# Performance work log

Measured on AMD Instinct MI355X. Metric: run time of the kernel, lower is better.

## Reference

```python
import jax, jax.numpy as jnp
import numpy as np

INPUT_DIMS = 512
OUTPUT_DIMS = 512
GRID_SIZE = 8


def setup_inputs() -> dict:
    key = jax.random.key(0)
    k_x, k_w = jax.random.split(key)
    x = jax.random.normal(k_x, (4, 2048, INPUT_DIMS), dtype=jnp.float32)
    scale = 1.0 / (np.sqrt(INPUT_DIMS) * np.sqrt(GRID_SIZE))
    fouriercoeffs = jax.random.normal(
        k_w, (2, OUTPUT_DIMS, INPUT_DIMS, GRID_SIZE), dtype=jnp.float32) * scale
    bias = jnp.zeros((1, OUTPUT_DIMS), dtype=jnp.float32)
    return {"x": x, "fouriercoeffs": fouriercoeffs, "bias": bias}


def reference(x, fouriercoeffs, bias):
    out_shape = x.shape[:-1] + (OUTPUT_DIMS,)
    xf = x.reshape(-1, INPUT_DIMS)  # [N, I]
    k = jnp.arange(1, GRID_SIZE + 1, dtype=x.dtype)  # [G]
    arg = xf[:, :, None] * k  # [N, I, G]
    # contract cos/sin features against coeffs: two batched GEMMs
    y = jnp.einsum('nig,oig->no', jnp.cos(arg), fouriercoeffs[0])
    y = y + jnp.einsum('nig,oig->no', jnp.sin(arg), fouriercoeffs[1])
    y = y + bias
    return y.reshape(out_shape)
```

## Files before the change

### kernel.cpp

```cpp
#include <hip/hip_runtime.h>
#include <hip/hip_bf16.h>


typedef __attribute__((ext_vector_type(8)))  short s16x8;
typedef __attribute__((ext_vector_type(4)))  int   i32x4;
typedef __attribute__((ext_vector_type(4)))  float f32x4;
typedef __attribute__((ext_vector_type(16))) float f32x16;

#define NROWS 8192
#define IDIM  512
#define ODIM  512
#define KDIM  8192

static __device__ __forceinline__ short f2bf(float f) {
    union { float f; unsigned u; } v; v.f = f;
    unsigned r = v.u + 0x7fffu + ((v.u >> 16) & 1u);
    return (short)(r >> 16);
}

static __device__ __forceinline__ float bf2f(short h) {
    union { unsigned u; float f; } v;
    v.u = ((unsigned)(unsigned short)h) << 16;
    return v.f;
}

static __device__ __forceinline__ int pkbf(float c, float s) {
    union { __hip_bfloat162 h; int i; } u;
    u.h = __float22bfloat162_rn(make_float2(c, s));
    return u.i;
}

__global__ __launch_bounds__(256) void fkan_prep(const float* __restrict__ cf,
                                                 short* __restrict__ Wb) {
    const int o = blockIdx.x;
    const int tid = threadIdx.x;
#pragma unroll
    for (int rep = 0; rep < 2; ++rep) {
        const int i = tid + rep * 256;
        const float* c0 = cf + (o * 512 + i) * 8;
        const float* c1 = cf + ((512 + o) * 512 + i) * 8;
        float4 a0 = *(const float4*)c0;
        float4 a1 = *(const float4*)(c0 + 4);
        float4 b0 = *(const float4*)c1;
        float4 b1 = *(const float4*)(c1 + 4);
        s16x8 lo, hi;
        lo[0] = f2bf(a0.x); lo[1] = f2bf(b0.x);
        lo[2] = f2bf(a0.y); lo[3] = f2bf(b0.y);
        lo[4] = f2bf(a0.z); lo[5] = f2bf(b0.z);
        lo[6] = f2bf(a0.w); lo[7] = f2bf(b0.w);
        hi[0] = f2bf(a1.x); hi[1] = f2bf(b1.x);
        hi[2] = f2bf(a1.y); hi[3] = f2bf(b1.y);
        hi[4] = f2bf(a1.z); hi[5] = f2bf(b1.z);
        hi[6] = f2bf(a1.w); hi[7] = f2bf(b1.w);
        *(s16x8*)(Wb + o * KDIM + i * 16)     = lo;
        *(s16x8*)(Wb + o * KDIM + i * 16 + 8) = hi;
    }
}

__global__ __launch_bounds__(256, 2) void fkan_gemm10(const float* __restrict__ x,
                                                      const short* __restrict__ Wb,
                                                      short* __restrict__ P) {
    __shared__ short As[2][64 * 64];
    __shared__ short Bs[2][128 * 64];

    const int bid = blockIdx.x;
    const int xcd = bid & 7;
    const int bn = xcd & 1, kc = xcd >> 1;
    const int bm = bid >> 3;
    const int n0 = bm * 128, o0 = bn * 256, i0 = kc * 128;
    const int kbase = i0 * 16;
    const int NKT = 64;

    const int tid = threadIdx.x;
    const int wid = tid >> 6, lane = tid & 63;
    const int l32 = lane & 31, hi32 = lane >> 5;
    const int wr = wid >> 1, wc = wid & 1;

    f32x16 acc[2][4];
#pragma unroll
    for (int a = 0; a < 2; ++a)
#pragma unroll
        for (int b = 0; b < 4; ++b)
#pragma unroll
            for (int e = 0; e < 16; ++e) acc[a][b][e] = 0.f;

    const int nl = tid >> 1, isel = tid & 1;
    const float* xrow = x + (n0 + nl) * 512 + i0 + isel;

    auto stage = [&](int t, int nb, float xx) {
#pragma unroll
        for (int w = 0; w < 4; ++w) {
            const int ch = w * 256 + tid;
            const int l = ch >> 3, sl = ch & 7;
            const int cb = sl ^ (l & 7);
            const int r = 2 * l + (cb >> 2);
            const short* src = Wb + (size_t)(o0 + r) * KDIM + kbase + t * 32 + (cb & 3) * 8;
            short* ldst = &Bs[nb][w * 2048 + wid * 512];
            __builtin_amdgcn_global_load_lds(
                (const __attribute__((address_space(1))) void*)src,
                (__attribute__((address_space(3))) void*)ldst, 16, 0, 0);
        }
        float s1, c1;
        __sincosf(xx, &s1, &c1);
        float c = c1, s = s1;
        i32x4 lo, hi;
#pragma unroll
        for (int g = 0; g < 8; ++g) {
            const int p = pkbf(c, s);
            if (g < 4) lo[g] = p; else hi[g - 4] = p;
            const float t1 = s * s1, t2 = c * s1;
            const float cn = __builtin_fmaf(c, c1, -t1);
            s = __builtin_fmaf(s, c1, t2);
            c = cn;
        }
        short* Ab = As[nb];
        const int lA = nl >> 1;
        const int cb0 = (nl & 1) * 4 + isel * 2;
        *(i32x4*)&Ab[lA * 64 + ((cb0 ^ (lA & 7))) * 8]       = lo;
        *(i32x4*)&Ab[lA * 64 + (((cb0 + 1) ^ (lA & 7))) * 8] = hi;
    };

    float xv = xrow[0];
    stage(0, 0, xv);
    xv = xrow[2];
    __syncthreads();

    for (int kt = 0; kt < NKT; ++kt) {
        const int cur = kt & 1;

        s16x8 af[2][2], bfr[4][2];
#pragma unroll
        for (int mt = 0; mt < 2; ++mt)
#pragma unroll
            for (int ks = 0; ks < 2; ++ks) {
                const int row = wr * 64 + mt * 32 + l32;
                const int cch = ks * 2 + hi32;
                const int l = row >> 1;
                const int slot = (((row & 1) * 4 + cch) ^ (l & 7));
                af[mt][ks] = *(const s16x8*)&As[cur][l * 64 + slot * 8];
            }
#pragma unroll
        for (int nt = 0; nt < 4; ++nt)
#pragma unroll
            for (int ks = 0; ks < 2; ++ks) {
                const int row = wc * 128 + nt * 32 + l32;
                const int cch = ks * 2 + hi32;
                const int l = row >> 1;
                const int slot = (((row & 1) * 4 + cch) ^ (l & 7));
                bfr[nt][ks] = *(const s16x8*)&Bs[cur][l * 64 + slot * 8];
            }

        if (kt + 1 < NKT) {
            stage(kt + 1, cur ^ 1, xv);
            if (kt + 2 < NKT) xv = xrow[(kt + 2) * 2];
        }

#pragma unroll
        for (int ks = 0; ks < 2; ++ks)
#pragma unroll
            for (int mt = 0; mt < 2; ++mt)
#pragma unroll
                for (int nt = 0; nt < 4; ++nt)
                    acc[mt][nt] = __builtin_amdgcn_mfma_f32_32x32x16_bf16(
                        af[mt][ks], bfr[nt][ks], acc[mt][nt], 0, 0, 0);

        __syncthreads();
    }

    unsigned short* dst = (unsigned short*)P + (size_t)kc * (NROWS * ODIM);
#pragma unroll
    for (int mt = 0; mt < 2; ++mt)
#pragma unroll
        for (int nt = 0; nt < 4; ++nt) {
            const f32x16 v = acc[mt][nt];
            const int oc = o0 + wc * 128 + nt * 32 + l32;
            const int rb = n0 + wr * 64 + mt * 32 + 4 * hi32;
#pragma unroll
            for (int reg = 0; reg < 16; ++reg) {
                const int row = rb + (reg & 3) + 8 * (reg >> 2);
                dst[(size_t)row * 512 + oc] = (unsigned short)f2bf(v[reg]);
            }
        }
}

__global__ __launch_bounds__(256) void fkan_combine4(const short* __restrict__ P,
                                                     const float* __restrict__ bias,
                                                     float* __restrict__ out) {
    const int total = NROWS * ODIM;
    const int stride = gridDim.x * 256 * 8;
    for (int e = (blockIdx.x * 256 + threadIdx.x) * 8; e < total; e += stride) {
        s16x8 a = *(const s16x8*)(P + e);
        s16x8 b = *(const s16x8*)(P + total + e);
        s16x8 c = *(const s16x8*)(P + 2 * total + e);
        s16x8 d = *(const s16x8*)(P + 3 * total + e);
        const int col = e & 511;
        float4 c0 = *(const float4*)(bias + col);
        float4 c1 = *(const float4*)(bias + col + 4);
        float4 r0, r1;
        r0.x = (bf2f(a[0]) + bf2f(b[0])) + (bf2f(c[0]) + bf2f(d[0])) + c0.x;
        r0.y = (bf2f(a[1]) + bf2f(b[1])) + (bf2f(c[1]) + bf2f(d[1])) + c0.y;
        r0.z = (bf2f(a[2]) + bf2f(b[2])) + (bf2f(c[2]) + bf2f(d[2])) + c0.z;
        r0.w = (bf2f(a[3]) + bf2f(b[3])) + (bf2f(c[3]) + bf2f(d[3])) + c0.w;
        r1.x = (bf2f(a[4]) + bf2f(b[4])) + (bf2f(c[4]) + bf2f(d[4])) + c1.x;
        r1.y = (bf2f(a[5]) + bf2f(b[5])) + (bf2f(c[5]) + bf2f(d[5])) + c1.y;
        r1.z = (bf2f(a[6]) + bf2f(b[6])) + (bf2f(c[6]) + bf2f(d[6])) + c1.z;
        r1.w = (bf2f(a[7]) + bf2f(b[7])) + (bf2f(c[7]) + bf2f(d[7])) + c1.w;
        *(float4*)(out + e)     = r0;
        *(float4*)(out + e + 4) = r1;
    }
}

__global__ __launch_bounds__(256, 2) void fkan_gemm_fb(const float* __restrict__ x,
                                                       const short* __restrict__ Wb,
                                                       const float* __restrict__ bias,
                                                       float* __restrict__ outp) {
    __shared__ short As[2][128 * 64];
    __shared__ short Bs[2][128 * 64];
    const int bid = blockIdx.x;
    const int xcd = bid & 7, idx = bid >> 3;
    const int bn = xcd & 3, bm = idx + (xcd >> 2) * 32;
    const int n0 = bm * 128, o0 = bn * 128;
    const int tid = threadIdx.x;
    const int wid = tid >> 6, lane = tid & 63;
    const int lrow = lane & 15, lk = lane >> 4;
    const int wr = wid >> 1, wc = wid & 1;
    f32x4 acc[4][4];
#pragma unroll
    for (int a = 0; a < 4; ++a)
#pragma unroll
        for (int b = 0; b < 4; ++b) { f32x4 z = {0,0,0,0}; acc[a][b] = z; }
    const int nl = tid >> 1, isel = tid & 1;
    const float* xrow = x + (n0 + nl) * 512 + isel * 2;
    auto stage = [&](int t, int nb, float2 xvv) {
#pragma unroll
        for (int w = 0; w < 4; ++w) {
            const int chunk = w * 256 + tid;
            const int r = chunk >> 3, pc = chunk & 7;
            const int lc = pc ^ (r & 7);
            const short* src = Wb + (o0 + r) * KDIM + t * 64 + lc * 8;
            short* ldst = &Bs[nb][w * 2048 + wid * 512];
            __builtin_amdgcn_global_load_lds(
                (const __attribute__((address_space(1))) void*)src,
                (__attribute__((address_space(3))) void*)ldst, 16, 0, 0);
        }
#pragma unroll
        for (int ii = 0; ii < 2; ++ii) {
            const float xx = ii ? xvv.y : xvv.x;
            float s1, c1; __sincosf(xx, &s1, &c1);
            float c = c1, s = s1;
            i32x4 lo, hi;
#pragma unroll
            for (int g = 0; g < 8; ++g) {
                const int p = pkbf(c, s);
                if (g < 4) lo[g] = p; else hi[g - 4] = p;
                const float t1 = s * s1, t2 = c * s1;
                const float cn = __builtin_fmaf(c, c1, -t1);
                s = __builtin_fmaf(s, c1, t2); c = cn;
            }
            const int cb0 = (isel * 2 + ii) * 2;
            *(i32x4*)&As[nb][nl * 64 + ((cb0 ^ (nl & 7))) * 8]       = lo;
            *(i32x4*)&As[nb][nl * 64 + (((cb0 + 1) ^ (nl & 7))) * 8] = hi;
        }
    };
    float2 xv = *(const float2*)xrow;
    stage(0, 0, xv);
    xv = *(const float2*)(xrow + 4);
    __syncthreads();
    for (int kt = 0; kt < 128; ++kt) {
        const int cur = kt & 1;
        s16x8 af[2][4], bfr[2][4];
#pragma unroll
        for (int ksub = 0; ksub < 2; ++ksub) {
#pragma unroll
            for (int mf = 0; mf < 4; ++mf) {
                const int row = wr * 64 + mf * 16 + lrow;
                af[ksub][mf] = *(const s16x8*)&As[cur][row * 64 + ((ksub * 4 + lk) ^ (row & 7)) * 8];
            }
#pragma unroll
            for (int nf = 0; nf < 4; ++nf) {
                const int row = wc * 64 + nf * 16 + lrow;
                bfr[ksub][nf] = *(const s16x8*)&Bs[cur][row * 64 + ((ksub * 4 + lk) ^ (row & 7)) * 8];
            }
        }
        if (kt + 1 < 128) {
            stage(kt + 1, cur ^ 1, xv);
            if (kt + 2 < 128) xv = *(const float2*)(xrow + (kt + 2) * 4);
        }
#pragma unroll
        for (int ksub = 0; ksub < 2; ++ksub)
#pragma unroll
            for (int mf = 0; mf < 4; ++mf)
#pragma unroll
                for (int nf = 0; nf < 4; ++nf)
                    acc[mf][nf] = __builtin_amdgcn_mfma_f32_16x16x32_bf16(
                        af[ksub][mf], bfr[ksub][nf], acc[mf][nf], 0, 0, 0);
        __syncthreads();
    }
#pragma unroll
    for (int nf = 0; nf < 4; ++nf) {
        const int oc = o0 + wc * 64 + nf * 16 + lrow;
        const float bv = bias[oc];
#pragma unroll
        for (int mf = 0; mf < 4; ++mf) {
            const f32x4 v = acc[mf][nf];
            const int rbase = n0 + wr * 64 + mf * 16 + lk * 4;
#pragma unroll
            for (int j = 0; j < 4; ++j)
                outp[(size_t)(rbase + j) * 512 + oc] = v[j] + bv;
        }
    }
}

extern "C" void kernel_launch(void* const* d_in, const int* in_sizes, int n_in,
                              void* d_out, int out_size, void* d_ws, size_t ws_size,
                              hipStream_t stream) {
    const float* x    = (const float*)d_in[0];
    const float* cf   = (const float*)d_in[1];
    const float* bias = (const float*)d_in[2];
    float* out = (float*)d_out;

    const size_t partial_bytes = (size_t)4 * NROWS * ODIM * 2;
    const size_t wb_bytes = (size_t)ODIM * KDIM * 2;

    if (ws_size >= partial_bytes + wb_bytes) {
        short* P  = (short*)d_ws;
        short* Wb = (short*)((char*)d_ws + partial_bytes);
        fkan_prep<<<512, 256, 0, stream>>>(cf, Wb);
        fkan_gemm10<<<512, 256, 0, stream>>>(x, Wb, P);
        fkan_combine4<<<2048, 256, 0, stream>>>(P, bias, out);
    } else {
        short* Wb = (short*)d_ws;
        fkan_prep<<<512, 256, 0, stream>>>(cf, Wb);
        fkan_gemm_fb<<<256, 256, 0, stream>>>(x, Wb, bias, out);
    }
}
```

Baseline: 96.32 us.

## Build A-operand Fourier fragments in registers via permlane swap, drop A LDS tile

Instead of computing cos/sin features cooperatively and staging them through shared memory, each lane now computes the A-operand MFMA fragments for its own rows directly in registers. It uses v_permlane32_swap to rearrange the packed bf16 values into the fragment layout. This removes the A tile from LDS along with its writes and reads. The cost is that the sincos and recurrence work is duplicated, since the two wave columns covering the same rows each redo it, and the per-iteration x loads are now strided scalar loads.

```diff
diff --git a/kernel.cpp b/kernel.cpp
--- a/kernel.cpp
+++ b/kernel.cpp
@@ -57,10 +57,9 @@
     }
 }
 
-__global__ __launch_bounds__(256, 2) void fkan_gemm10(const float* __restrict__ x,
+__global__ __launch_bounds__(256, 2) void fkan_gemm11(const float* __restrict__ x,
                                                       const short* __restrict__ Wb,
                                                       short* __restrict__ P) {
-    __shared__ short As[2][64 * 64];
     __shared__ short Bs[2][128 * 64];
 
     const int bid = blockIdx.x;
@@ -84,10 +83,9 @@
 #pragma unroll
             for (int e = 0; e < 16; ++e) acc[a][b][e] = 0.f;
 
-    const int nl = tid >> 1, isel = tid & 1;
-    const float* xrow = x + (n0 + nl) * 512 + i0 + isel;
-
-    auto stage = [&](int t, int nb, float xx) {
+    const float* xlane = x + (size_t)(n0 + wr * 64 + l32) * 512 + i0 + hi32;
+
+    auto stageB = [&](int t, int nb) {
 #pragma unroll
         for (int w = 0; w < 4; ++w) {
             const int ch = w * 256 + tid;
@@ -100,59 +98,61 @@
                 (const __attribute__((address_space(1))) void*)src,
                 (__attribute__((address_space(3))) void*)ldst, 16, 0, 0);
         }
+    };
+
+    auto buildA = [&](float xx, s16x8& f0, s16x8& f1) {
         float s1, c1;
         __sincosf(xx, &s1, &c1);
         float c = c1, s = s1;
-        i32x4 lo, hi;
+        int I[8];
 #pragma unroll
         for (int g = 0; g < 8; ++g) {
-            const int p = pkbf(c, s);
-            if (g < 4) lo[g] = p; else hi[g - 4] = p;
+            I[g] = pkbf(c, s);
             const float t1 = s * s1, t2 = c * s1;
             const float cn = __builtin_fmaf(c, c1, -t1);
             s = __builtin_fmaf(s, c1, t2);
             c = cn;
         }
-        short* Ab = As[nb];
-        const int lA = nl >> 1;
-        const int cb0 = (nl & 1) * 4 + isel * 2;
-        *(i32x4*)&Ab[lA * 64 + ((cb0 ^ (lA & 7))) * 8]       = lo;
-        *(i32x4*)&Ab[lA * 64 + (((cb0 + 1) ^ (lA & 7))) * 8] = hi;
+        i32x4 a0, a1;
+#pragma unroll
+        for (int j = 0; j < 4; ++j) {
+            int va = I[j], vb = I[j + 4];
+            asm volatile("v_permlane32_swap_b32 %0, %1" : "+v"(va), "+v"(vb));
+            a0[j] = va; a1[j] = vb;
+        }
+        f0 = *(s16x8*)&a0;
+        f1 = *(s16x8*)&a1;
     };
 
-    float xv = xrow[0];
-    stage(0, 0, xv);
-    xv = xrow[2];
+    float xv0 = xlane[0];
+    float xv1 = xlane[32 * 512];
+    stageB(0, 0);
     __syncthreads();
 
     for (int kt = 0; kt < NKT; ++kt) {
         const int cur = kt & 1;
-
-        s16x8 af[2][2], bfr[4][2];
-#pragma unroll
-        for (int mt = 0; mt < 2; ++mt)
-#pragma unroll
-            for (int ks = 0; ks < 2; ++ks) {
-                const int row = wr * 64 + mt * 32 + l32;
-                const int cch = ks * 2 + hi32;
-                const int l = row >> 1;
-                const int slot = (((row & 1) * 4 + cch) ^ (l & 7));
-                af[mt][ks] = *(const s16x8*)&As[cur][l * 64 + slot * 8];
-            }
+        const short* Bcur = Bs[cur];
+
+        if (kt + 1 < NKT) stageB(kt + 1, cur ^ 1);
+
+        s16x8 bfr[4][2];
 #pragma unroll
         for (int nt = 0; nt < 4; ++nt)
 #pragma unroll
             for (int ks = 0; ks < 2; ++ks) {
                 const int row = wc * 128 + nt * 32 + l32;
-                const int cch = ks * 2 + hi32;
                 const int l = row >> 1;
-                const int slot = (((row & 1) * 4 + cch) ^ (l & 7));
-                bfr[nt][ks] = *(const s16x8*)&Bs[cur][l * 64 + slot * 8];
-            }
+                const int slot = (((row & 1) * 4 + ks * 2 + hi32) ^ (l & 7));
+                bfr[nt][ks] = *(const s16x8*)&Bcur[l * 64 + slot * 8];
+            }
+
+        s16x8 af[2][2];
+        buildA(xv0, af[0][0], af[0][1]);
+        buildA(xv1, af[1][0], af[1][1]);
 
         if (kt + 1 < NKT) {
-            stage(kt + 1, cur ^ 1, xv);
-            if (kt + 2 < NKT) xv = xrow[(kt + 2) * 2];
+            xv0 = xlane[(kt + 1) * 2];
+            xv1 = xlane[32 * 512 + (kt + 1) * 2];
         }
 
 #pragma unroll
@@ -326,7 +326,7 @@
         short* P  = (short*)d_ws;
         short* Wb = (short*)((char*)d_ws + partial_bytes);
         fkan_prep<<<512, 256, 0, stream>>>(cf, Wb);
-        fkan_gemm10<<<512, 256, 0, stream>>>(x, Wb, P);
+        fkan_gemm11<<<512, 256, 0, stream>>>(x, Wb, P);
         fkan_combine4<<<2048, 256, 0, stream>>>(P, bias, out);
     } else {
         short* Wb = (short*)d_ws;
```

New measurement: 115.5 us. 19.9% more time.

## Halve GEMM M-tile to 64 rows and double grid for higher occupancy

Applied to the files above, without the earlier changes.

The split-K GEMM tile shrinks from 128 to 64 rows per block. The grid doubles to 1024 blocks and launch bounds move from 2 to 4 blocks per CU. Each wave now holds one M-subtile of accumulators, which roughly halves accumulator registers. Only half the threads compute the sin/cos features, and global and LDS addresses are precomputed outside the K loop. The K loop is unrolled by two and its MFMAs are split into two stages to interleave LDS reads with compute. The cost is lower arithmetic intensity: each weight tile is fetched twice as many times, so L2 and HBM traffic for the weights rises.

```diff
diff --git a/kernel.cpp b/kernel.cpp
--- a/kernel.cpp
+++ b/kernel.cpp
@@ -57,17 +57,17 @@
     }
 }
 
-__global__ __launch_bounds__(256, 2) void fkan_gemm10(const float* __restrict__ x,
+__global__ __launch_bounds__(256, 4) void fkan_gemm12(const float* __restrict__ x,
                                                       const short* __restrict__ Wb,
                                                       short* __restrict__ P) {
-    __shared__ short As[2][64 * 64];
-    __shared__ short Bs[2][128 * 64];
+    __shared__ short As[2][64 * 32];
+    __shared__ short Bs[2][256 * 32];
 
     const int bid = blockIdx.x;
     const int xcd = bid & 7;
     const int bn = xcd & 1, kc = xcd >> 1;
     const int bm = bid >> 3;
-    const int n0 = bm * 128, o0 = bn * 256, i0 = kc * 128;
+    const int n0 = bm * 64, o0 = bn * 256, i0 = kc * 128;
     const int kbase = i0 * 16;
     const int NKT = 64;
 
@@ -76,111 +76,119 @@
     const int l32 = lane & 31, hi32 = lane >> 5;
     const int wr = wid >> 1, wc = wid & 1;
 
-    f32x16 acc[2][4];
-#pragma unroll
-    for (int a = 0; a < 2; ++a)
-#pragma unroll
-        for (int b = 0; b < 4; ++b)
-#pragma unroll
-            for (int e = 0; e < 16; ++e) acc[a][b][e] = 0.f;
-
-    const int nl = tid >> 1, isel = tid & 1;
-    const float* xrow = x + (n0 + nl) * 512 + i0 + isel;
+    f32x16 acc[4];
+#pragma unroll
+    for (int b = 0; b < 4; ++b)
+#pragma unroll
+        for (int e = 0; e < 16; ++e) acc[b][e] = 0.f;
+
+    const bool stg = (tid & 1) == 0;
+    const int srow = tid >> 2;
+    const int sisel = (tid >> 1) & 1;
+    const float* xsrc = x + (size_t)(n0 + srow) * 512 + i0 + sisel;
+    const int slin = srow >> 1;
+    const int scb0 = (srow & 1) * 4 + sisel * 2;
+    const int sAo0 = slin * 64 + ((scb0 ^ (slin & 7))) * 8;
+    const int sAo1 = slin * 64 + (((scb0 + 1) ^ (slin & 7))) * 8;
+
+    const short* bsrc[4];
+#pragma unroll
+    for (int w = 0; w < 4; ++w) {
+        const int ch = w * 256 + tid;
+        const int l = ch >> 3, sl = ch & 7;
+        const int cb = sl ^ (l & 7);
+        const int r = 2 * l + (cb >> 2);
+        bsrc[w] = Wb + (size_t)(o0 + r) * KDIM + kbase + (cb & 3) * 8;
+    }
+
+    const int arow = wr * 32 + l32;
+    const int alin = arow >> 1;
+    int aoff[2];
+#pragma unroll
+    for (int ks = 0; ks < 2; ++ks)
+        aoff[ks] = alin * 64 + ((((arow & 1) << 2) + ks * 2 + hi32) ^ (alin & 7)) * 8;
+    const int brow = wc * 128 + l32;
+    const int blin = brow >> 1;
+    int boff[2];
+#pragma unroll
+    for (int ks = 0; ks < 2; ++ks)
+        boff[ks] = blin * 64 + ((((brow & 1) << 2) + ks * 2 + hi32) ^ (blin & 7)) * 8;
 
     auto stage = [&](int t, int nb, float xx) {
 #pragma unroll
         for (int w = 0; w < 4; ++w) {
-            const int ch = w * 256 + tid;
-            const int l = ch >> 3, sl = ch & 7;
-            const int cb = sl ^ (l & 7);
-            const int r = 2 * l + (cb >> 2);
-            const short* src = Wb + (size_t)(o0 + r) * KDIM + kbase + t * 32 + (cb & 3) * 8;
             short* ldst = &Bs[nb][w * 2048 + wid * 512];
             __builtin_amdgcn_global_load_lds(
-                (const __attribute__((address_space(1))) void*)src,
+                (const __attribute__((address_space(1))) void*)(bsrc[w] + t * 32),
                 (__attribute__((address_space(3))) void*)ldst, 16, 0, 0);
         }
-        float s1, c1;
-        __sincosf(xx, &s1, &c1);
-        float c = c1, s = s1;
-        i32x4 lo, hi;
-#pragma unroll
-        for (int g = 0; g < 8; ++g) {
-            const int p = pkbf(c, s);
-            if (g < 4) lo[g] = p; else hi[g - 4] = p;
-            const float t1 = s * s1, t2 = c * s1;
-            const float cn = __builtin_fmaf(c, c1, -t1);
-            s = __builtin_fmaf(s, c1, t2);
-            c = cn;
-        }
-        short* Ab = As[nb];
-        const int lA = nl >> 1;
-        const int cb0 = (nl & 1) * 4 + isel * 2;
-        *(i32x4*)&Ab[lA * 64 + ((cb0 ^ (lA & 7))) * 8]       = lo;
-        *(i32x4*)&Ab[lA * 64 + (((cb0 + 1) ^ (lA & 7))) * 8] = hi;
+        if (stg) {
+            float s1, c1;
+            __sincosf(xx, &s1, &c1);
+            float c = c1, s = s1;
+            i32x4 lo, hi;
+#pragma unroll
+            for (int g = 0; g < 8; ++g) {
+                const int p = pkbf(c, s);
+                if (g < 4) lo[g] = p; else hi[g - 4] = p;
+                const float t1 = s * s1, t2 = c * s1;
+                const float cn = __builtin_fmaf(c, c1, -t1);
+                s = __builtin_fmaf(s, c1, t2);
+                c = cn;
+            }
+            *(i32x4*)&As[nb][sAo0] = lo;
+            *(i32x4*)&As[nb][sAo1] = hi;
+        }
     };
 
-    float xv = xrow[0];
+    float xv = xsrc[0];
     stage(0, 0, xv);
-    xv = xrow[2];
+    xv = xsrc[2];
     __syncthreads();
 
+#pragma unroll 2
     for (int kt = 0; kt < NKT; ++kt) {
         const int cur = kt & 1;
 
-        s16x8 af[2][2], bfr[4][2];
-#pragma unroll
-        for (int mt = 0; mt < 2; ++mt)
-#pragma unroll
-            for (int ks = 0; ks < 2; ++ks) {
-                const int row = wr * 64 + mt * 32 + l32;
-                const int cch = ks * 2 + hi32;
-                const int l = row >> 1;
-                const int slot = (((row & 1) * 4 + cch) ^ (l & 7));
-                af[mt][ks] = *(const s16x8*)&As[cur][l * 64 + slot * 8];
-            }
+        s16x8 af0 = *(const s16x8*)&As[cur][aoff[0]];
+        s16x8 af1 = *(const s16x8*)&As[cur][aoff[1]];
+        s16x8 b0[4];
 #pragma unroll
         for (int nt = 0; nt < 4; ++nt)
-#pragma unroll
-            for (int ks = 0; ks < 2; ++ks) {
-                const int row = wc * 128 + nt * 32 + l32;
-                const int cch = ks * 2 + hi32;
-                const int l = row >> 1;
-                const int slot = (((row & 1) * 4 + cch) ^ (l & 7));
-                bfr[nt][ks] = *(const s16x8*)&Bs[cur][l * 64 + slot * 8];
-            }
+            b0[nt] = *(const s16x8*)&Bs[cur][boff[0] + nt * 1024];
 
         if (kt + 1 < NKT) {
             stage(kt + 1, cur ^ 1, xv);
-            if (kt + 2 < NKT) xv = xrow[(kt + 2) * 2];
-        }
-
-#pragma unroll
-        for (int ks = 0; ks < 2; ++ks)
-#pragma unroll
-            for (int mt = 0; mt < 2; ++mt)
-#pragma unroll
-                for (int nt = 0; nt < 4; ++nt)
-                    acc[mt][nt] = __builtin_amdgcn_mfma_f32_32x32x16_bf16(
-                        af[mt][ks], bfr[nt][ks], acc[mt][nt], 0, 0, 0);
+            if (kt + 2 < NKT) xv = xsrc[(kt + 2) * 2];
+        }
+
+#pragma unroll
+        for (int nt = 0; nt < 4; ++nt)
+            acc[nt] = __builtin_amdgcn_mfma_f32_32x32x16_bf16(af0, b0[nt], acc[nt], 0, 0, 0);
+
+        s16x8 b1[4];
+#pragma unroll
+        for (int nt = 0; nt < 4; ++nt)
+            b1[nt] = *(const s16x8*)&Bs[cur][boff[1] + nt * 1024];
+#pragma unroll
+        for (int nt = 0; nt < 4; ++nt)
+            acc[nt] = __builtin_amdgcn_mfma_f32_32x32x16_bf16(af1, b1[nt], acc[nt], 0, 0, 0);
 
         __syncthreads();
     }
 
     unsigned short* dst = (unsigned short*)P + (size_t)kc * (NROWS * ODIM);
 #pragma unroll
-    for (int mt = 0; mt < 2; ++mt)
-#pragma unroll
-        for (int nt = 0; nt < 4; ++nt) {
-            const f32x16 v = acc[mt][nt];
-            const int oc = o0 + wc * 128 + nt * 32 + l32;
-            const int rb = n0 + wr * 64 + mt * 32 + 4 * hi32;
-#pragma unroll
-            for (int reg = 0; reg < 16; ++reg) {
-                const int row = rb + (reg & 3) + 8 * (reg >> 2);
-                dst[(size_t)row * 512 + oc] = (unsigned short)f2bf(v[reg]);
-            }
-        }
+    for (int nt = 0; nt < 4; ++nt) {
+        const f32x16 v = acc[nt];
+        const int oc = o0 + wc * 128 + nt * 32 + l32;
+        const int rb = n0 + wr * 32 + 4 * hi32;
+#pragma unroll
+        for (int reg = 0; reg < 16; ++reg) {
+            const int row = rb + (reg & 3) + 8 * (reg >> 2);
+            dst[(size_t)row * 512 + oc] = (unsigned short)f2bf(v[reg]);
+        }
+    }
 }
 
 __global__ __launch_bounds__(256) void fkan_combine4(const short* __restrict__ P,
@@ -326,7 +334,7 @@
         short* P  = (short*)d_ws;
         short* Wb = (short*)((char*)d_ws + partial_bytes);
         fkan_prep<<<512, 256, 0, stream>>>(cf, Wb);
-        fkan_gemm10<<<512, 256, 0, stream>>>(x, Wb, P);
+        fkan_gemm12<<<1024, 256, 0, stream>>>(x, Wb, P);
         fkan_combine4<<<2048, 256, 0, stream>>>(P, bias, out);
     } else {
         short* Wb = (short*)d_ws;
```

Result: slower. 124.3 us (+29.1%).
